# Kernel optimization log

Hardware: AMD Instinct MI355X
Metric: run time of the kernel (lower is better)

## Reference

```python
import jax, jax.numpy as jnp
import numpy as np

SEQ, N, D, E = 16, 50000, 128, 1600000  # seq_len, n_nodes (lstm batch), feature dim, n_edges


def setup_inputs() -> dict:
    key = jax.random.key(0)
    ks = jax.random.split(key, 12)
    s = 1.0 / np.sqrt(D)

    def unif(k, shape):
        return jax.random.uniform(k, shape, jnp.float32, -s, s)

    return {
        "input_aux": jax.random.normal(ks[0], (SEQ, N, D), jnp.float32),
        "edges": jax.random.randint(ks[1], (2, E), 0, N, dtype=jnp.int64),
        # PyTorch LSTM params (single layer): gates ordered [i, f, g, o]
        "W_ih": unif(ks[2], (4 * D, D)),
        "W_hh": unif(ks[3], (4 * D, D)),
        "b_ih": unif(ks[4], (4 * D,)),
        "b_hh": unif(ks[5], (4 * D,)),
        # GCNConv layers (normalize=False): x' = scatter_sum((x @ W)[src] -> dst) + b
        "W1": unif(ks[6], (D, D)),
        "b1": unif(ks[7], (D,)),
        "W2": unif(ks[8], (D, D)),
        "b2": unif(ks[9], (D,)),
    }


def _lstm_last_hidden(x, W_ih, W_hh, b_ih, b_hh):
    # x: [T, N, D] (batch_first=False). Returns final hidden state h_T: [N, H].
    H = W_hh.shape[1]
    b = b_ih + b_hh

    def step(carry, xt):
        h, c = carry
        gates = xt @ W_ih.T + h @ W_hh.T + b  # [N, 4H]
        i, f, g, o = jnp.split(gates, 4, axis=-1)
        i = jax.nn.sigmoid(i)
        f = jax.nn.sigmoid(f)
        g = jnp.tanh(g)
        o = jax.nn.sigmoid(o)
        c = f * c + i * g
        h = o * jnp.tanh(c)
        return (h, c), None

    h0 = jnp.zeros((x.shape[1], H), x.dtype)
    (h, _), _ = jax.lax.scan(step, (h0, h0), x)
    return h


def _gcn_conv(x, edges, W, b):
    # GCNConv with normalize=False: transform, gather from source, scatter-sum to target, add bias.
    xw = x @ W                                    # [N, D]
    msg = xw[edges[0]]                            # [E, D] gather
    out = jax.ops.segment_sum(msg, edges[1], num_segments=x.shape[0])  # [N, D] scatter
    return out + b


def reference(input_aux, W_ih, W_hh, b_ih, b_hh, W1, b1, W2, b2, edges):
    h = _lstm_last_hidden(input_aux, W_ih, W_hh, b_ih, b_hh)  # squeeze(hn): [N, D]
    x = jax.nn.relu(_gcn_conv(h, edges, W1, b1))
    return _gcn_conv(x, edges, W2, b2)
```

## Files before the change

kernel.cpp:

```cpp
#include <hip/hip_runtime.h>
#include <hip/hip_bf16.h>

#define D 128
#define G4 512
#define KK 256

typedef __attribute__((ext_vector_type(4))) float f32x4;
typedef __attribute__((ext_vector_type(8))) __bf16 bf16x8;
typedef __attribute__((ext_vector_type(8))) unsigned short u16x8;

__device__ __forceinline__ float sigm2(float x) {
    return __builtin_amdgcn_rcpf(1.0f + __builtin_amdgcn_exp2f(-1.4426950408889634f * x));
}
__device__ __forceinline__ float tanh2(float x) {
    return 1.0f - 2.0f * __builtin_amdgcn_rcpf(1.0f + __builtin_amdgcn_exp2f(2.8853900817779268f * x));
}
__device__ __forceinline__ float bf_lo(unsigned int u) { return __uint_as_float(u << 16); }
__device__ __forceinline__ float bf_hi(unsigned int u) { return __uint_as_float(u & 0xffff0000u); }

__global__ void k_prep(const float* __restrict__ Wih, const float* __restrict__ Whh,
                       const float* __restrict__ bih, const float* __restrict__ bhh,
                       const float* __restrict__ W1, const float* __restrict__ W2,
                       __bf16* __restrict__ Wcomb, __bf16* __restrict__ W1t,
                       __bf16* __restrict__ W2t, float* __restrict__ bcomb) {
    int t = blockIdx.x * blockDim.x + threadIdx.x;
    if (t < G4 * KK) {
        int row = t / KK, k = t % KK;
        float v = (k < D) ? Wih[row * D + k] : Whh[row * D + (k - D)];
        Wcomb[t] = (__bf16)v;
    } else if (t < G4 * KK + D * D) {
        int u = t - G4 * KK; int o = u / D, k = u % D;
        W1t[u] = (__bf16)W1[k * D + o];
    } else if (t < G4 * KK + 2 * D * D) {
        int u = t - G4 * KK - D * D; int o = u / D, k = u % D;
        W2t[u] = (__bf16)W2[k * D + o];
    } else if (t < G4 * KK + 2 * D * D + G4) {
        int u = t - G4 * KK - 2 * D * D;
        bcomb[u] = bih[u] + bhh[u];
    }
}

__global__ __launch_bounds__(512, 2) void k_lstm2(
        const float* __restrict__ xin, const __bf16* __restrict__ Wcomb,
        const float* __restrict__ bcomb, const __bf16* __restrict__ W1t,
        __bf16* __restrict__ xw1, int n, int tsteps, int nchunks) {
    __shared__ float  gbuf[16][516];
    __shared__ __bf16 xbuf[16][D];
    __shared__ __bf16 hbuf[16][D];

    const int tid = threadIdx.x;
    const int wid = tid >> 6, l = tid & 63, q = l >> 4, c16 = l & 15;
    const int dim = wid * 16 + c16;

    bf16x8 Wf[4][8];
#pragma unroll
    for (int ct = 0; ct < 4; ++ct)
#pragma unroll
        for (int kb = 0; kb < 8; ++kb)
            Wf[ct][kb] = *(const bf16x8*)(Wcomb + (size_t)(wid * 64 + ct * 16 + c16) * KK + kb * 32 + q * 8);

    const float bI = bcomb[0 * D + dim], bF = bcomb[1 * D + dim],
                bG = bcomb[2 * D + dim], bO = bcomb[3 * D + dim];

    const int srow = tid >> 4, sc8 = (tid & 15) * 8;

    for (int chunk = blockIdx.x; chunk < nchunks; chunk += gridDim.x) {
        const int R = chunk * 16;
        float cst[4] = {0.f, 0.f, 0.f, 0.f};

        if (tid < 256) {
            ((float4*)hbuf)[tid] = make_float4(0.f, 0.f, 0.f, 0.f);
            const float* xp = xin + ((size_t)(R + srow)) * D + sc8;
            float4 v0 = *(const float4*)xp, v1 = *(const float4*)(xp + 4);
            bf16x8 b;
            b[0] = (__bf16)v0.x; b[1] = (__bf16)v0.y; b[2] = (__bf16)v0.z; b[3] = (__bf16)v0.w;
            b[4] = (__bf16)v1.x; b[5] = (__bf16)v1.y; b[6] = (__bf16)v1.z; b[7] = (__bf16)v1.w;
            *(bf16x8*)&xbuf[srow][sc8 ^ ((srow & 7) << 3)] = b;
        }
        __syncthreads();

        for (int t = 0; t < tsteps; ++t) {
            float4 p0, p1;
            const bool pf = (t + 1 < tsteps) && (tid < 256);
            if (pf) {
                const float* xp = xin + ((size_t)(t + 1) * n + R + srow) * D + sc8;
                p0 = *(const float4*)xp; p1 = *(const float4*)(xp + 4);
            }

            bf16x8 a[8];
#pragma unroll
            for (int kb = 0; kb < 4; ++kb)
                a[kb] = *(const bf16x8*)&xbuf[c16][(kb * 32 + q * 8) ^ ((c16 & 7) << 3)];
#pragma unroll
            for (int kb = 0; kb < 4; ++kb)
                a[4 + kb] = *(const bf16x8*)&hbuf[c16][(kb * 32 + q * 8) ^ ((c16 & 7) << 3)];

            f32x4 acc[4] = {{0,0,0,0},{0,0,0,0},{0,0,0,0},{0,0,0,0}};
#pragma unroll
            for (int kb = 0; kb < 8; ++kb)
#pragma unroll
                for (int ct = 0; ct < 4; ++ct)
                    acc[ct] = __builtin_amdgcn_mfma_f32_16x16x32_bf16(a[kb], Wf[ct][kb], acc[ct], 0, 0, 0);

#pragma unroll
            for (int ct = 0; ct < 4; ++ct)
#pragma unroll
                for (int j = 0; j < 4; ++j)
                    gbuf[q * 4 + j][wid * 64 + ct * 16 + c16] = acc[ct][j];
            __syncthreads();

#pragma unroll
            for (int j = 0; j < 4; ++j) {
                const int node = q * 4 + j;
                float gi = gbuf[node][0 * D + dim];
                float gf = gbuf[node][1 * D + dim];
                float gg = gbuf[node][2 * D + dim];
                float go = gbuf[node][3 * D + dim];
                float iv = sigm2(gi + bI);
                float fv = sigm2(gf + bF);
                float gv = tanh2(gg + bG);
                float ov = sigm2(go + bO);
                float c = fv * cst[j] + iv * gv;
                cst[j] = c;
                float h = ov * tanh2(c);
                hbuf[node][dim ^ ((node & 7) << 3)] = (__bf16)h;
            }
            if (pf) {
                bf16x8 b;
                b[0] = (__bf16)p0.x; b[1] = (__bf16)p0.y; b[2] = (__bf16)p0.z; b[3] = (__bf16)p0.w;
                b[4] = (__bf16)p1.x; b[5] = (__bf16)p1.y; b[6] = (__bf16)p1.z; b[7] = (__bf16)p1.w;
                *(bf16x8*)&xbuf[srow][sc8 ^ ((srow & 7) << 3)] = b;
            }
            __syncthreads();
        }

        f32x4 acc1 = {0, 0, 0, 0};
#pragma unroll
        for (int kb = 0; kb < 4; ++kb) {
            bf16x8 a = *(const bf16x8*)&hbuf[c16][(kb * 32 + q * 8) ^ ((c16 & 7) << 3)];
            bf16x8 wf = *(const bf16x8*)(W1t + (size_t)(wid * 16 + c16) * D + kb * 32 + q * 8);
            acc1 = __builtin_amdgcn_mfma_f32_16x16x32_bf16(a, wf, acc1, 0, 0, 0);
        }
#pragma unroll
        for (int j = 0; j < 4; ++j)
            xw1[(size_t)(R + q * 4 + j) * D + wid * 16 + c16] = (__bf16)acc1[j];
        __syncthreads();
    }
}

__global__ __launch_bounds__(256) void k_gemm2(
        const __bf16* __restrict__ in, const __bf16* __restrict__ Wt,
        __bf16* __restrict__ outm, int n) {
    const int tid = threadIdx.x, wid = tid >> 6, l = tid & 63, q = l >> 4, c16 = l & 15;
    const int R = (blockIdx.x * 4 + wid) * 16;
    if (R + 16 > n) return;
    bf16x8 af[4];
#pragma unroll
    for (int kb = 0; kb < 4; ++kb) {
        u16x8 v = *(const u16x8*)((const unsigned short*)in + (size_t)(R + c16) * D + kb * 32 + q * 8);
#pragma unroll
        for (int j = 0; j < 8; ++j)
            if (v[j] & 0x8000u) v[j] = 0;
        af[kb] = *(bf16x8*)&v;
    }
#pragma unroll
    for (int nt = 0; nt < 8; ++nt) {
        f32x4 acc = {0, 0, 0, 0};
#pragma unroll
        for (int kb = 0; kb < 4; ++kb) {
            const __bf16* wb = Wt + (size_t)(nt * 16 + c16) * D + (kb * 32 + q * 8);
            acc = __builtin_amdgcn_mfma_f32_16x16x32_bf16(af[kb], *(const bf16x8*)wb, acc, 0, 0, 0);
        }
#pragma unroll
        for (int j = 0; j < 4; ++j)
            outm[(size_t)(R + q * 4 + j) * D + nt * 16 + c16] = (__bf16)acc[j];
    }
}

__global__ void k_zero(int* p, int n) {
    int i = blockIdx.x * blockDim.x + threadIdx.x;
    if (i < n) p[i] = 0;
}
__global__ void k_hist(const int* __restrict__ dst, int* __restrict__ counts, int e) {
    for (int i = blockIdx.x * blockDim.x + threadIdx.x; i < e; i += gridDim.x * blockDim.x)
        atomicAdd(&counts[dst[i]], 1);
}
__global__ __launch_bounds__(1024) void k_scan1(const int* __restrict__ counts,
        int* __restrict__ offsets, int* __restrict__ bsum, int n) {
    __shared__ int sd[1024];
    int tid = threadIdx.x, i = blockIdx.x * 1024 + tid;
    int v = (i < n) ? counts[i] : 0;
    sd[tid] = v; __syncthreads();
    for (int off = 1; off < 1024; off <<= 1) {
        int t = (tid >= off) ? sd[tid - off] : 0; __syncthreads();
        sd[tid] += t; __syncthreads();
    }
    if (i < n) offsets[i] = sd[tid] - v;
    if (tid == 1023) bsum[blockIdx.x] = sd[1023];
}
__global__ void k_scan2(const int* __restrict__ bsum, int* __restrict__ bpref, int nb) {
    if (threadIdx.x == 0) {
        int run = 0;
        for (int i = 0; i < nb; ++i) { bpref[i] = run; run += bsum[i]; }
    }
}
__global__ __launch_bounds__(1024) void k_scan3(int* __restrict__ offsets,
        int* __restrict__ cursor, const int* __restrict__ bpref, int n, int e) {
    int i = blockIdx.x * 1024 + threadIdx.x;
    if (i < n) {
        int v = offsets[i] + bpref[blockIdx.x];
        offsets[i] = v; cursor[i] = v;
    }
    if (i == 0) offsets[n] = e;
}
__global__ void k_permute(const int* __restrict__ src, const int* __restrict__ dst,
                          int* cursor, int* __restrict__ csr, int e) {
    for (int i = blockIdx.x * blockDim.x + threadIdx.x; i < e; i += gridDim.x * blockDim.x) {
        int p = atomicAdd(&cursor[dst[i]], 1);
        csr[p] = src[i];
    }
}

template <bool OUT_F32>
__global__ __launch_bounds__(256) void k_gather2(const __bf16* __restrict__ xw,
        const int* __restrict__ offsets, const int* __restrict__ csr,
        const float* __restrict__ bias, void* __restrict__ outp, int n) {
    int wid = threadIdx.x >> 6, l = threadIdx.x & 63;
    int d = blockIdx.x * 4 + wid;
    if (d >= n) return;
    int s = offsets[d], e = offsets[d + 1];
    const unsigned int* xu = (const unsigned int*)xw;
    float a0 = 0.f, a1 = 0.f;
    int i = s;
    for (; i + 4 <= e; i += 4) {
        unsigned int u0 = xu[(size_t)csr[i]     * 64 + l];
        unsigned int u1 = xu[(size_t)csr[i + 1] * 64 + l];
        unsigned int u2 = xu[(size_t)csr[i + 2] * 64 + l];
        unsigned int u3 = xu[(size_t)csr[i + 3] * 64 + l];
        a0 += (bf_lo(u0) + bf_lo(u1)) + (bf_lo(u2) + bf_lo(u3));
        a1 += (bf_hi(u0) + bf_hi(u1)) + (bf_hi(u2) + bf_hi(u3));
    }
    for (; i < e; ++i) {
        unsigned int u = xu[(size_t)csr[i] * 64 + l];
        a0 += bf_lo(u); a1 += bf_hi(u);
    }
    float2 bb = *(const float2*)(bias + 2 * l);
    float r0 = a0 + bb.x, r1 = a1 + bb.y;
    if (OUT_F32) {
        float2* o = (float2*)outp;
        o[(size_t)d * 64 + l] = make_float2(r0, r1);
    } else {
        __bf16* o = (__bf16*)outp;
        o[(size_t)d * D + 2 * l]     = (__bf16)r0;
        o[(size_t)d * D + 2 * l + 1] = (__bf16)r1;
    }
}

extern "C" void kernel_launch(void* const* d_in, const int* in_sizes, int n_in,
                              void* d_out, int out_size, void* d_ws, size_t ws_size,
                              hipStream_t stream) {
    const float* xin = (const float*)d_in[0];
    const int*   edges = (const int*)d_in[1];
    const float* Wih = (const float*)d_in[2];
    const float* Whh = (const float*)d_in[3];
    const float* bih = (const float*)d_in[4];
    const float* bhh = (const float*)d_in[5];
    const float* W1  = (const float*)d_in[6];
    const float* b1  = (const float*)d_in[7];
    const float* W2  = (const float*)d_in[8];
    const float* b2  = (const float*)d_in[9];
    float* outp = (float*)d_out;

    const int E = in_sizes[1] / 2;
    const int n = out_size / D;
    const int tsteps = in_sizes[0] / (n * D);
    const int* srcE = edges;
    const int* dstE = edges + E;

    char* ws = (char*)d_ws;
    size_t off = 0;
    auto alloc = [&](size_t bytes) { void* p = ws + off; off += (bytes + 511) & ~(size_t)511; return p; };
    __bf16* Wcomb = (__bf16*)alloc((size_t)G4 * KK * 2);
    __bf16* W1t   = (__bf16*)alloc((size_t)D * D * 2);
    __bf16* W2t   = (__bf16*)alloc((size_t)D * D * 2);
    float*  bcomb = (float*)alloc((size_t)G4 * 4);
    int* counts  = (int*)alloc((size_t)(n + 1) * 4);
    int* offsets = (int*)alloc((size_t)(n + 1) * 4);
    int* cursor  = (int*)alloc((size_t)(n + 1) * 4);
    int* bsum    = (int*)alloc(64 * 4);
    int* bpref   = (int*)alloc(64 * 4);
    int* csr     = (int*)alloc((size_t)E * 4);
    __bf16* xw1  = (__bf16*)alloc((size_t)n * D * 2);
    __bf16* out1 = (__bf16*)alloc((size_t)n * D * 2);
    __bf16* xw2  = xw1;
    (void)ws_size; (void)n_in;

    {
        int total = G4 * KK + 2 * D * D + G4;
        k_prep<<<(total + 255) / 256, 256, 0, stream>>>(Wih, Whh, bih, bhh, W1, W2,
                                                        Wcomb, W1t, W2t, bcomb);
    }
    k_zero<<<(n + 255) / 256, 256, 0, stream>>>(counts, n);
    k_hist<<<2048, 256, 0, stream>>>(dstE, counts, E);
    int nb = (n + 1023) / 1024;
    k_scan1<<<nb, 1024, 0, stream>>>(counts, offsets, bsum, n);
    k_scan2<<<1, 64, 0, stream>>>(bsum, bpref, nb);
    k_scan3<<<nb, 1024, 0, stream>>>(offsets, cursor, bpref, n, E);
    k_permute<<<2048, 256, 0, stream>>>(srcE, dstE, cursor, csr, E);

    k_lstm2<<<256, 512, 0, stream>>>(xin, Wcomb, bcomb, W1t, xw1, n, tsteps, n / 16);

    k_gather2<false><<<(n + 3) / 4, 256, 0, stream>>>(xw1, offsets, csr, b1, out1, n);
    k_gemm2<<<((n / 16) + 3) / 4, 256, 0, stream>>>(out1, W2t, xw2, n);
    k_gather2<true><<<(n + 3) / 4, 256, 0, stream>>>(xw2, offsets, csr, b2, outp, n);
}
```

Baseline: 1.105 ms.

## Process two node chunks per LSTM block and widen gather to 16-byte loads

The LSTM kernel now handles two 16-node chunks per block. Each wave keeps all four gates of its own hidden dims in registers, so the gate activations are computed straight from the MFMA accumulators without the shared gate buffer and its extra barrier. x and h are double-buffered, leaving one barrier per step. The gather kernel uses 16 lanes per node with 128-bit loads and fuses the ReLU, so the ReLU masking in the second GEMM goes away. The zero kernel is also replaced by a memset. The trade-offs are higher register pressure (occupancy bound drops to 1) and fewer gathers in flight per lane.

Measured after the change: 1.043 ms. -5.6%, faster.

```diff
diff --git a/kernel.cpp b/kernel.cpp
--- a/kernel.cpp
+++ b/kernel.cpp
@@ -8,6 +8,7 @@
 typedef __attribute__((ext_vector_type(4))) float f32x4;
 typedef __attribute__((ext_vector_type(8))) __bf16 bf16x8;
 typedef __attribute__((ext_vector_type(8))) unsigned short u16x8;
+typedef __attribute__((ext_vector_type(4))) unsigned int u32x4;
 
 __device__ __forceinline__ float sigm2(float x) {
     return __builtin_amdgcn_rcpf(1.0f + __builtin_amdgcn_exp2f(-1.4426950408889634f * x));
@@ -40,13 +41,12 @@
     }
 }
 
-__global__ __launch_bounds__(512, 2) void k_lstm2(
+__global__ __launch_bounds__(512, 1) void k_lstm3(
         const float* __restrict__ xin, const __bf16* __restrict__ Wcomb,
         const float* __restrict__ bcomb, const __bf16* __restrict__ W1t,
-        __bf16* __restrict__ xw1, int n, int tsteps, int nchunks) {
-    __shared__ float  gbuf[16][516];
-    __shared__ __bf16 xbuf[16][D];
-    __shared__ __bf16 hbuf[16][D];
+        __bf16* __restrict__ xw1, int n, int tsteps, int npairs, int nchunks) {
+    __shared__ __bf16 xb[2][2][16][D];
+    __shared__ __bf16 hb[2][2][16][D];
 
     const int tid = threadIdx.x;
     const int wid = tid >> 6, l = tid & 63, q = l >> 4, c16 = l & 15;
@@ -54,96 +54,130 @@
 
     bf16x8 Wf[4][8];
 #pragma unroll
-    for (int ct = 0; ct < 4; ++ct)
+    for (int g = 0; g < 4; ++g)
 #pragma unroll
         for (int kb = 0; kb < 8; ++kb)
-            Wf[ct][kb] = *(const bf16x8*)(Wcomb + (size_t)(wid * 64 + ct * 16 + c16) * KK + kb * 32 + q * 8);
+            Wf[g][kb] = *(const bf16x8*)(Wcomb + (size_t)(g * D + dim) * KK + kb * 32 + q * 8);
+#pragma unroll
+    for (int g = 0; g < 4; ++g)
+#pragma unroll
+        for (int kb = 0; kb < 8; ++kb) {
+            f32x4 tmp = __builtin_bit_cast(f32x4, Wf[g][kb]);
+            asm volatile("" : "+v"(tmp));
+            Wf[g][kb] = __builtin_bit_cast(bf16x8, tmp);
+        }
 
     const float bI = bcomb[0 * D + dim], bF = bcomb[1 * D + dim],
                 bG = bcomb[2 * D + dim], bO = bcomb[3 * D + dim];
 
-    const int srow = tid >> 4, sc8 = (tid & 15) * 8;
-
-    for (int chunk = blockIdx.x; chunk < nchunks; chunk += gridDim.x) {
-        const int R = chunk * 16;
-        float cst[4] = {0.f, 0.f, 0.f, 0.f};
-
-        if (tid < 256) {
-            ((float4*)hbuf)[tid] = make_float4(0.f, 0.f, 0.f, 0.f);
-            const float* xp = xin + ((size_t)(R + srow)) * D + sc8;
+    const int sid = tid >> 8;
+    const int su = tid & 255;
+    const int srow = su >> 4, sc8 = (su & 15) * 8;
+    const int fin = tsteps & 1;
+
+    for (int p = blockIdx.x; p < npairs; p += gridDim.x) {
+        const int cA = 2 * p, cB = 2 * p + 1;
+        const bool hasB = (cB < nchunks);
+        const int myc = sid ? (hasB ? cB : cA) : cA;
+
+        ((float4*)&hb[sid][0][0][0])[su] = make_float4(0.f, 0.f, 0.f, 0.f);
+        {
+            const float* xp = xin + ((size_t)(myc * 16 + srow)) * D + sc8;
             float4 v0 = *(const float4*)xp, v1 = *(const float4*)(xp + 4);
             bf16x8 b;
             b[0] = (__bf16)v0.x; b[1] = (__bf16)v0.y; b[2] = (__bf16)v0.z; b[3] = (__bf16)v0.w;
             b[4] = (__bf16)v1.x; b[5] = (__bf16)v1.y; b[6] = (__bf16)v1.z; b[7] = (__bf16)v1.w;
-            *(bf16x8*)&xbuf[srow][sc8 ^ ((srow & 7) << 3)] = b;
+            *(bf16x8*)&xb[sid][0][srow][sc8 ^ ((srow & 7) << 3)] = b;
         }
         __syncthreads();
 
+        float csA[4] = {0.f, 0.f, 0.f, 0.f}, csB[4] = {0.f, 0.f, 0.f, 0.f};
+
         for (int t = 0; t < tsteps; ++t) {
+            const int cur = t & 1, nxt = cur ^ 1;
+
+            bf16x8 aA[8], aB[8];
+#pragma unroll
+            for (int kb = 0; kb < 4; ++kb) {
+                const int e = (kb * 32 + q * 8) ^ ((c16 & 7) << 3);
+                aA[kb]     = *(const bf16x8*)&xb[0][cur][c16][e];
+                aA[4 + kb] = *(const bf16x8*)&hb[0][cur][c16][e];
+                aB[kb]     = *(const bf16x8*)&xb[1][cur][c16][e];
+                aB[4 + kb] = *(const bf16x8*)&hb[1][cur][c16][e];
+            }
+
             float4 p0, p1;
-            const bool pf = (t + 1 < tsteps) && (tid < 256);
+            const bool pf = (t + 1 < tsteps);
             if (pf) {
-                const float* xp = xin + ((size_t)(t + 1) * n + R + srow) * D + sc8;
+                const float* xp = xin + ((size_t)(t + 1) * n + myc * 16 + srow) * D + sc8;
                 p0 = *(const float4*)xp; p1 = *(const float4*)(xp + 4);
             }
 
-            bf16x8 a[8];
-#pragma unroll
-            for (int kb = 0; kb < 4; ++kb)
-                a[kb] = *(const bf16x8*)&xbuf[c16][(kb * 32 + q * 8) ^ ((c16 & 7) << 3)];
-#pragma unroll
-            for (int kb = 0; kb < 4; ++kb)
-                a[4 + kb] = *(const bf16x8*)&hbuf[c16][(kb * 32 + q * 8) ^ ((c16 & 7) << 3)];
-
-            f32x4 acc[4] = {{0,0,0,0},{0,0,0,0},{0,0,0,0},{0,0,0,0}};
+            f32x4 accA[4] = {{0,0,0,0},{0,0,0,0},{0,0,0,0},{0,0,0,0}};
+            f32x4 accB[4] = {{0,0,0,0},{0,0,0,0},{0,0,0,0},{0,0,0,0}};
 #pragma unroll
             for (int kb = 0; kb < 8; ++kb)
 #pragma unroll
-                for (int ct = 0; ct < 4; ++ct)
-                    acc[ct] = __builtin_amdgcn_mfma_f32_16x16x32_bf16(a[kb], Wf[ct][kb], acc[ct], 0, 0, 0);
-
-#pragma unroll
-            for (int ct = 0; ct < 4; ++ct)
-#pragma unroll
-                for (int j = 0; j < 4; ++j)
-                    gbuf[q * 4 + j][wid * 64 + ct * 16 + c16] = acc[ct][j];
-            __syncthreads();
-
-#pragma unroll
-            for (int j = 0; j < 4; ++j) {
-                const int node = q * 4 + j;
-                float gi = gbuf[node][0 * D + dim];
-                float gf = gbuf[node][1 * D + dim];
-                float gg = gbuf[node][2 * D + dim];
-                float go = gbuf[node][3 * D + dim];
-                float iv = sigm2(gi + bI);
-                float fv = sigm2(gf + bF);
-                float gv = tanh2(gg + bG);
-                float ov = sigm2(go + bO);
-                float c = fv * cst[j] + iv * gv;
-                cst[j] = c;
-                float h = ov * tanh2(c);
-                hbuf[node][dim ^ ((node & 7) << 3)] = (__bf16)h;
-            }
+                for (int g = 0; g < 4; ++g) {
+                    accA[g] = __builtin_amdgcn_mfma_f32_16x16x32_bf16(aA[kb], Wf[g][kb], accA[g], 0, 0, 0);
+                    accB[g] = __builtin_amdgcn_mfma_f32_16x16x32_bf16(aB[kb], Wf[g][kb], accB[g], 0, 0, 0);
+                }
+
             if (pf) {
                 bf16x8 b;
                 b[0] = (__bf16)p0.x; b[1] = (__bf16)p0.y; b[2] = (__bf16)p0.z; b[3] = (__bf16)p0.w;
                 b[4] = (__bf16)p1.x; b[5] = (__bf16)p1.y; b[6] = (__bf16)p1.z; b[7] = (__bf16)p1.w;
-                *(bf16x8*)&xbuf[srow][sc8 ^ ((srow & 7) << 3)] = b;
+                *(bf16x8*)&xb[sid][nxt][srow][sc8 ^ ((srow & 7) << 3)] = b;
+            }
+
+#pragma unroll
+            for (int j = 0; j < 4; ++j) {
+                const int node = j + q * 4;
+                {
+                    float iv = sigm2(accA[0][j] + bI);
+                    float fv = sigm2(accA[1][j] + bF);
+                    float gv = tanh2(accA[2][j] + bG);
+                    float ov = sigm2(accA[3][j] + bO);
+                    float c = fv * csA[j] + iv * gv;
+                    csA[j] = c;
+                    hb[0][nxt][node][dim ^ ((node & 7) << 3)] = (__bf16)(ov * tanh2(c));
+                }
+                {
+                    float iv = sigm2(accB[0][j] + bI);
+                    float fv = sigm2(accB[1][j] + bF);
+                    float gv = tanh2(accB[2][j] + bG);
+                    float ov = sigm2(accB[3][j] + bO);
+                    float c = fv * csB[j] + iv * gv;
+                    csB[j] = c;
+                    hb[1][nxt][node][dim ^ ((node & 7) << 3)] = (__bf16)(ov * tanh2(c));
+                }
             }
             __syncthreads();
         }
 
-        f32x4 acc1 = {0, 0, 0, 0};
+        bf16x8 hA[4], hB[4];
 #pragma unroll
         for (int kb = 0; kb < 4; ++kb) {
-            bf16x8 a = *(const bf16x8*)&hbuf[c16][(kb * 32 + q * 8) ^ ((c16 & 7) << 3)];
-            bf16x8 wf = *(const bf16x8*)(W1t + (size_t)(wid * 16 + c16) * D + kb * 32 + q * 8);
-            acc1 = __builtin_amdgcn_mfma_f32_16x16x32_bf16(a, wf, acc1, 0, 0, 0);
-        }
-#pragma unroll
-        for (int j = 0; j < 4; ++j)
-            xw1[(size_t)(R + q * 4 + j) * D + wid * 16 + c16] = (__bf16)acc1[j];
+            const int e = (kb * 32 + q * 8) ^ ((c16 & 7) << 3);
+            hA[kb] = *(const bf16x8*)&hb[0][fin][c16][e];
+            hB[kb] = *(const bf16x8*)&hb[1][fin][c16][e];
+        }
+        f32x4 eA = {0,0,0,0}, eB = {0,0,0,0};
+#pragma unroll
+        for (int kb = 0; kb < 4; ++kb) {
+            bf16x8 wf = *(const bf16x8*)(W1t + (size_t)dim * D + kb * 32 + q * 8);
+            eA = __builtin_amdgcn_mfma_f32_16x16x32_bf16(hA[kb], wf, eA, 0, 0, 0);
+            eB = __builtin_amdgcn_mfma_f32_16x16x32_bf16(hB[kb], wf, eB, 0, 0, 0);
+        }
+#pragma unroll
+        for (int j = 0; j < 4; ++j) {
+            const int node = j + q * 4;
+            xb[0][1][node][dim] = (__bf16)eA[j];
+            xb[1][1][node][dim] = (__bf16)eB[j];
+        }
+        __syncthreads();
+        if (!(sid == 1 && !hasB))
+            *(bf16x8*)(xw1 + (size_t)(myc * 16 + srow) * D + sc8) = *(const bf16x8*)&xb[sid][1][srow][sc8];
         __syncthreads();
     }
 }
@@ -156,13 +190,8 @@
     if (R + 16 > n) return;
     bf16x8 af[4];
 #pragma unroll
-    for (int kb = 0; kb < 4; ++kb) {
-        u16x8 v = *(const u16x8*)((const unsigned short*)in + (size_t)(R + c16) * D + kb * 32 + q * 8);
-#pragma unroll
-        for (int j = 0; j < 8; ++j)
-            if (v[j] & 0x8000u) v[j] = 0;
-        af[kb] = *(bf16x8*)&v;
-    }
+    for (int kb = 0; kb < 4; ++kb)
+        af[kb] = *(const bf16x8*)(in + (size_t)(R + c16) * D + kb * 32 + q * 8);
 #pragma unroll
     for (int nt = 0; nt < 8; ++nt) {
         f32x4 acc = {0, 0, 0, 0};
@@ -177,10 +206,6 @@
     }
 }
 
-__global__ void k_zero(int* p, int n) {
-    int i = blockIdx.x * blockDim.x + threadIdx.x;
-    if (i < n) p[i] = 0;
-}
 __global__ void k_hist(const int* __restrict__ dst, int* __restrict__ counts, int e) {
     for (int i = blockIdx.x * blockDim.x + threadIdx.x; i < e; i += gridDim.x * blockDim.x)
         atomicAdd(&counts[dst[i]], 1);
@@ -221,38 +246,50 @@
     }
 }
 
-template <bool OUT_F32>
-__global__ __launch_bounds__(256) void k_gather2(const __bf16* __restrict__ xw,
+template <bool OUT_F32, bool RELU>
+__global__ __launch_bounds__(256) void k_gather3(const __bf16* __restrict__ xw,
         const int* __restrict__ offsets, const int* __restrict__ csr,
         const float* __restrict__ bias, void* __restrict__ outp, int n) {
-    int wid = threadIdx.x >> 6, l = threadIdx.x & 63;
-    int d = blockIdx.x * 4 + wid;
-    if (d >= n) return;
-    int s = offsets[d], e = offsets[d + 1];
-    const unsigned int* xu = (const unsigned int*)xw;
-    float a0 = 0.f, a1 = 0.f;
+    const int gg = (blockIdx.x << 4) | (threadIdx.x >> 4);
+    const int l = threadIdx.x & 15;
+    if (gg >= n) return;
+    const int s = offsets[gg], e = offsets[gg + 1];
+    const u32x4* __restrict__ xq = (const u32x4*)xw;
+    float a[8] = {0,0,0,0,0,0,0,0};
     int i = s;
     for (; i + 4 <= e; i += 4) {
-        unsigned int u0 = xu[(size_t)csr[i]     * 64 + l];
-        unsigned int u1 = xu[(size_t)csr[i + 1] * 64 + l];
-        unsigned int u2 = xu[(size_t)csr[i + 2] * 64 + l];
-        unsigned int u3 = xu[(size_t)csr[i + 3] * 64 + l];
-        a0 += (bf_lo(u0) + bf_lo(u1)) + (bf_lo(u2) + bf_lo(u3));
-        a1 += (bf_hi(u0) + bf_hi(u1)) + (bf_hi(u2) + bf_hi(u3));
+        u32x4 v0 = xq[(size_t)csr[i]     * 16 + l];
+        u32x4 v1 = xq[(size_t)csr[i + 1] * 16 + l];
+        u32x4 v2 = xq[(size_t)csr[i + 2] * 16 + l];
+        u32x4 v3 = xq[(size_t)csr[i + 3] * 16 + l];
+#pragma unroll
+        for (int k = 0; k < 4; ++k) {
+            a[2 * k]     += (bf_lo(v0[k]) + bf_lo(v1[k])) + (bf_lo(v2[k]) + bf_lo(v3[k]));
+            a[2 * k + 1] += (bf_hi(v0[k]) + bf_hi(v1[k])) + (bf_hi(v2[k]) + bf_hi(v3[k]));
+        }
     }
     for (; i < e; ++i) {
-        unsigned int u = xu[(size_t)csr[i] * 64 + l];
-        a0 += bf_lo(u); a1 += bf_hi(u);
-    }
-    float2 bb = *(const float2*)(bias + 2 * l);
-    float r0 = a0 + bb.x, r1 = a1 + bb.y;
+        u32x4 v = xq[(size_t)csr[i] * 16 + l];
+#pragma unroll
+        for (int k = 0; k < 4; ++k) { a[2 * k] += bf_lo(v[k]); a[2 * k + 1] += bf_hi(v[k]); }
+    }
+    const float4 b0 = *(const float4*)(bias + l * 8);
+    const float4 b1 = *(const float4*)(bias + l * 8 + 4);
+    float r[8] = {a[0] + b0.x, a[1] + b0.y, a[2] + b0.z, a[3] + b0.w,
+                  a[4] + b1.x, a[5] + b1.y, a[6] + b1.z, a[7] + b1.w};
+    if (RELU) {
+#pragma unroll
+        for (int k = 0; k < 8; ++k) r[k] = fmaxf(r[k], 0.f);
+    }
     if (OUT_F32) {
-        float2* o = (float2*)outp;
-        o[(size_t)d * 64 + l] = make_float2(r0, r1);
+        float* o = (float*)outp + (size_t)gg * D + l * 8;
+        *(float4*)o       = make_float4(r[0], r[1], r[2], r[3]);
+        *(float4*)(o + 4) = make_float4(r[4], r[5], r[6], r[7]);
     } else {
-        __bf16* o = (__bf16*)outp;
-        o[(size_t)d * D + 2 * l]     = (__bf16)r0;
-        o[(size_t)d * D + 2 * l + 1] = (__bf16)r1;
+        bf16x8 b;
+#pragma unroll
+        for (int k = 0; k < 8; ++k) b[k] = (__bf16)r[k];
+        *(bf16x8*)((__bf16*)outp + (size_t)gg * D + l * 8) = b;
     }
 }
 
@@ -300,7 +337,7 @@
         k_prep<<<(total + 255) / 256, 256, 0, stream>>>(Wih, Whh, bih, bhh, W1, W2,
                                                         Wcomb, W1t, W2t, bcomb);
     }
-    k_zero<<<(n + 255) / 256, 256, 0, stream>>>(counts, n);
+    hipMemsetAsync(counts, 0, (size_t)n * 4, stream);
     k_hist<<<2048, 256, 0, stream>>>(dstE, counts, E);
     int nb = (n + 1023) / 1024;
     k_scan1<<<nb, 1024, 0, stream>>>(counts, offsets, bsum, n);
@@ -308,9 +345,11 @@
     k_scan3<<<nb, 1024, 0, stream>>>(offsets, cursor, bpref, n, E);
     k_permute<<<2048, 256, 0, stream>>>(srcE, dstE, cursor, csr, E);
 
-    k_lstm2<<<256, 512, 0, stream>>>(xin, Wcomb, bcomb, W1t, xw1, n, tsteps, n / 16);
-
-    k_gather2<false><<<(n + 3) / 4, 256, 0, stream>>>(xw1, offsets, csr, b1, out1, n);
+    const int nchunks = n / 16;
+    const int npairs = (nchunks + 1) / 2;
+    k_lstm3<<<256, 512, 0, stream>>>(xin, Wcomb, bcomb, W1t, xw1, n, tsteps, npairs, nchunks);
+
+    k_gather3<false, true><<<(n + 15) / 16, 256, 0, stream>>>(xw1, offsets, csr, b1, out1, n);
     k_gemm2<<<((n / 16) + 3) / 4, 256, 0, stream>>>(out1, W2t, xw2, n);
-    k_gather2<true><<<(n + 3) / 4, 256, 0, stream>>>(xw2, offsets, csr, b2, outp, n);
-}
+    k_gather3<true, false><<<(n + 15) / 16, 256, 0, stream>>>(xw2, offsets, csr, b2, outp, n);
+}
```
